# Performance work log

Measured on AMD Instinct MI355X. Metric: run time of the kernel, lower is better.

## Reference

```python
import jax, jax.numpy as jnp
import numpy as np

B, N, DIM, H, K = 2, 8192, 256, 8, 32
HD = DIM // H


def setup_inputs() -> dict:
    key = jax.random.key(0)
    ks = jax.random.split(key, 10)
    s = 1.0 / np.sqrt(DIM)
    return {
        "x": jax.random.normal(ks[0], (B, N, DIM), jnp.float32),
        "xyz": jax.random.normal(ks[1], (B, N, 3), jnp.float32),
        "idx": jax.random.randint(ks[2], (B, N, K), 0, N, jnp.int32),
        "Wq": jax.random.normal(ks[3], (DIM, DIM), jnp.float32) * s,
        "bq": jnp.zeros((DIM,), jnp.float32),
        "Wk": jax.random.normal(ks[4], (DIM, DIM), jnp.float32) * s,
        "bk": jnp.zeros((DIM,), jnp.float32),
        "Wv": jax.random.normal(ks[5], (DIM, DIM), jnp.float32) * s,
        "bv": jnp.zeros((DIM,), jnp.float32),
        "Wo": jax.random.normal(ks[6], (DIM, DIM), jnp.float32) * s,
        "bo": jnp.zeros((DIM,), jnp.float32),
        "W1": jax.random.normal(ks[7], (3, 32), jnp.float32) * 0.5,
        "b1": jnp.zeros((32,), jnp.float32),
        "W2": jax.random.normal(ks[8], (32, H), jnp.float32) * 0.2,
        "b2": jnp.zeros((H,), jnp.float32),
    }


def reference(x, xyz, idx, Wq, bq, Wk, bk, Wv, bv, Wo, bo, W1, b1, W2, b2):
    Bn, Nn, C = x.shape
    k = idx.shape[-1]
    q = (x @ Wq + bq).reshape(Bn, Nn, H, HD)          # [B,N,H,hd]
    kf = (x @ Wk + bk).reshape(Bn, Nn, H, HD)
    vf = (x @ Wv + bv).reshape(Bn, Nn, H, HD)
    # gather k neighbors per point (per-batch fancy indexing)
    gather = jax.vmap(lambda f, i: f[i])               # [N,H,hd],[N,k] -> [N,k,H,hd]
    kn = gather(kf, idx)                               # [B,N,k,H,hd]
    vn = gather(vf, idx)
    nxyz = jax.vmap(lambda p, i: p[i])(xyz, idx)       # [B,N,k,3]
    rel = xyz[:, :, None, :] - nxyz                    # [B,N,k,3]
    bias = jax.nn.relu(rel @ W1 + b1) @ W2 + b2        # [B,N,k,H]
    scores = jnp.einsum('bnhd,bnkhd->bnhk', q, kn) / np.sqrt(HD).astype(np.float32)
    scores = scores + bias.transpose(0, 1, 3, 2)       # [B,N,H,k]
    attn = jax.nn.softmax(scores, axis=-1)
    out = jnp.einsum('bnhk,bnkhd->bnhd', attn, vn).reshape(Bn, Nn, C)
    return out @ Wo + bo
```

## Files before the change

kernel.cpp:

```cpp
#include <hip/hip_runtime.h>
#include <hip/hip_bf16.h>

typedef unsigned int uint32;
typedef unsigned short ushort;
typedef __attribute__((ext_vector_type(4))) float floatx4;
typedef __attribute__((ext_vector_type(8))) __bf16 bf16x8;

#define NPTS 8192
#define HSZ 524288

__device__ __forceinline__ ushort f2bf(float f) {
    uint32 u = __float_as_uint(f);
    uint32 r = (u + 0x7fffu + ((u >> 16) & 1u)) >> 16;
    return (ushort)r;
}
__device__ __forceinline__ float bf1(ushort u) { return __uint_as_float((uint32)u << 16); }
__device__ __forceinline__ float bflo(uint32 u) { return __uint_as_float(u << 16); }
__device__ __forceinline__ float bfhi(uint32 u) { return __uint_as_float(u & 0xffff0000u); }

__global__ __launch_bounds__(256) void prep_kernel(
    const float* __restrict__ x, const float* __restrict__ xyz, const int* __restrict__ idx,
    const float* __restrict__ Wq, const float* __restrict__ Wk,
    const float* __restrict__ Wv, const float* __restrict__ Wo,
    const float* __restrict__ bq, const float* __restrict__ bk, const float* __restrict__ bv,
    const float* __restrict__ W1, const float* __restrict__ b1,
    const float* __restrict__ W2, const float* __restrict__ b2,
    ushort* __restrict__ xb, ushort* __restrict__ Wqkvt, ushort* __restrict__ Wot,
    float* __restrict__ biasqkv, ushort* __restrict__ bias_hg) {
    const int bi = blockIdx.x;
    const int tid = threadIdx.x;
    if (bi < 4096) {
        int i = (bi * 256 + tid) * 4;
        float4 v = *(const float4*)(x + i);
        ushort4 o;
        o.x = f2bf(v.x); o.y = f2bf(v.y); o.z = f2bf(v.z); o.w = f2bf(v.w);
        *(ushort4*)(xb + i) = o;
    } else if (bi < 5120) {
        int f = (bi - 4096) * 256 + tid;
        if (f < 768 * 256) {
            int n = f >> 8, k = f & 255;
            int seg = n >> 8, nc = n & 255;
            const float* W = (seg == 0) ? Wq : (seg == 1) ? Wk : Wv;
            Wqkvt[f] = f2bf(W[k * 256 + nc]);
        } else {
            int g = f - 768 * 256;
            int n = g >> 8, k = g & 255;
            Wot[g] = f2bf(Wo[k * 256 + n]);
        }
        if (f < 768) biasqkv[f] = (f < 256) ? bq[f] : (f < 512) ? bk[f - 256] : bv[f - 512];
    } else {
        __shared__ float W1s[96], b1s[32], W2s[256], b2s[8];
        if (tid < 96) W1s[tid] = W1[tid];
        if (tid < 32) b1s[tid] = b1[tid];
        W2s[tid] = W2[tid];
        if (tid < 8) b2s[tid] = b2[tid];
        __syncthreads();
        const int wid = tid >> 6, lane = tid & 63;
        const int s = lane >> 5, j = lane & 31;
        const int p = (bi - 5120) * 8 + wid * 2 + s;
        const int b = p >> 13, n = p & 8191;
        const int nj = idx[(size_t)p * 32 + j];
        const size_t pb = ((size_t)b * NPTS + n) * 3;
        const size_t nb = ((size_t)b * NPTS + nj) * 3;
        const float rx = xyz[pb + 0] - xyz[nb + 0];
        const float ry = xyz[pb + 1] - xyz[nb + 1];
        const float rz = xyz[pb + 2] - xyz[nb + 2];
        float acc[8];
#pragma unroll
        for (int h = 0; h < 8; ++h) acc[h] = b2s[h];
#pragma unroll
        for (int u = 0; u < 32; ++u) {
            float hv = rx * W1s[u] + ry * W1s[32 + u] + rz * W1s[64 + u] + b1s[u];
            hv = fmaxf(hv, 0.f);
#pragma unroll
            for (int h = 0; h < 8; ++h) acc[h] += hv * W2s[u * 8 + h];
        }
#pragma unroll
        for (int h = 0; h < 8; ++h) bias_hg[(size_t)h * HSZ + p * 32 + j] = f2bf(acc[h]);
    }
}

__global__ __launch_bounds__(256) void gemm_qkv(const ushort* __restrict__ A,
                                                const ushort* __restrict__ Wt,
                                                const float* __restrict__ bias,
                                                ushort* __restrict__ qh, ushort* __restrict__ kh,
                                                ushort* __restrict__ vh) {
    __shared__ __align__(16) ushort As[128 * 64];
    __shared__ __align__(16) ushort Bs[128 * 64];
    const int tid = threadIdx.x;
    const int w = tid >> 6, lane = tid & 63;
    const int m0 = blockIdx.y * 128, n0 = blockIdx.x * 128;
    const int wm = (w & 1) * 64, wn = (w >> 1) * 64;

    floatx4 acc[4][4] = {};

    for (int kt = 0; kt < 256; kt += 64) {
        __syncthreads();
#pragma unroll
        for (int c4 = 0; c4 < 4; ++c4) {
            const int c = w * 4 + c4;
            const int r = c * 8 + (lane >> 3);
            const int gseg = (lane & 7) ^ (r & 7);
            const char* ga = (const char*)(A + (size_t)(m0 + r) * 256 + kt) + gseg * 16;
            const char* gb = (const char*)(Wt + (size_t)(n0 + r) * 256 + kt) + gseg * 16;
            __builtin_amdgcn_global_load_lds((const __attribute__((address_space(1))) void*)ga,
                                             (__attribute__((address_space(3))) void*)((char*)As + c * 1024),
                                             16, 0, 0);
            __builtin_amdgcn_global_load_lds((const __attribute__((address_space(1))) void*)gb,
                                             (__attribute__((address_space(3))) void*)((char*)Bs + c * 1024),
                                             16, 0, 0);
        }
        __syncthreads();

        bf16x8 af[2][4], bg[2][4];
#pragma unroll
        for (int kk = 0; kk < 2; ++kk) {
            const int s = kk * 4 + (lane >> 4);
            const int phys = s ^ (lane & 7);
#pragma unroll
            for (int i = 0; i < 4; ++i) {
                af[kk][i] = *(const bf16x8*)((const char*)As + (wm + i * 16 + (lane & 15)) * 128 + phys * 16);
                bg[kk][i] = *(const bf16x8*)((const char*)Bs + (wn + i * 16 + (lane & 15)) * 128 + phys * 16);
            }
        }
#pragma unroll
        for (int kk = 0; kk < 2; ++kk)
#pragma unroll
            for (int mi = 0; mi < 4; ++mi)
#pragma unroll
                for (int ni = 0; ni < 4; ++ni)
                    acc[mi][ni] = __builtin_amdgcn_mfma_f32_16x16x32_bf16(af[kk][mi], bg[kk][ni], acc[mi][ni], 0, 0, 0);
    }

#pragma unroll
    for (int ni = 0; ni < 4; ++ni) {
        const int col = n0 + wn + ni * 16 + (lane & 15);
        const int seg = col >> 8;
        const int head = (col >> 5) & 7;
        const int dim = col & 31;
        ushort* segp = (seg == 0) ? qh : (seg == 1) ? kh : vh;
        const float bv = bias[col];
#pragma unroll
        for (int mi = 0; mi < 4; ++mi) {
            const int row0 = m0 + wm + mi * 16 + (lane >> 4) * 4;
#pragma unroll
            for (int r = 0; r < 4; ++r)
                segp[(size_t)head * HSZ + (size_t)(row0 + r) * 32 + dim] = f2bf(acc[mi][ni][r] + bv);
        }
    }
}

__global__ __launch_bounds__(256) void gemm_mfma64(const ushort* __restrict__ A,
                                                   const ushort* __restrict__ Wt,
                                                   const float* __restrict__ bias,
                                                   float* __restrict__ outv, int N) {
    __shared__ __align__(16) ushort As[64 * 32];
    __shared__ __align__(16) ushort Bs[64 * 32];
    const int tid = threadIdx.x;
    const int w = tid >> 6, lane = tid & 63;
    const int m0 = blockIdx.y * 64, n0 = blockIdx.x * 64;
    const int row = tid >> 2;
    const int col16 = (tid & 3) * 16;

    floatx4 acc[4] = {};

    for (int kt = 0; kt < 256; kt += 32) {
        __syncthreads();
        {
            const char* ga = (const char*)(A + (size_t)(m0 + row) * 256 + kt) + col16;
            const char* gb = (const char*)(Wt + (size_t)(n0 + row) * 256 + kt) + col16;
            __builtin_amdgcn_global_load_lds((const __attribute__((address_space(1))) void*)ga,
                                             (__attribute__((address_space(3))) void*)((char*)As + w * 1024),
                                             16, 0, 0);
            __builtin_amdgcn_global_load_lds((const __attribute__((address_space(1))) void*)gb,
                                             (__attribute__((address_space(3))) void*)((char*)Bs + w * 1024),
                                             16, 0, 0);
        }
        __syncthreads();

        bf16x8 af = *(const bf16x8*)&As[(w * 16 + (lane & 15)) * 32 + (lane >> 4) * 8];
        bf16x8 bg[4];
#pragma unroll
        for (int ni = 0; ni < 4; ++ni)
            bg[ni] = *(const bf16x8*)&Bs[(ni * 16 + (lane & 15)) * 32 + (lane >> 4) * 8];
#pragma unroll
        for (int ni = 0; ni < 4; ++ni)
            acc[ni] = __builtin_amdgcn_mfma_f32_16x16x32_bf16(af, bg[ni], acc[ni], 0, 0, 0);
    }

#pragma unroll
    for (int ni = 0; ni < 4; ++ni) {
        const int col = n0 + ni * 16 + (lane & 15);
        const float bv = bias[col];
        const int row0 = m0 + w * 16 + (lane >> 4) * 4;
#pragma unroll
        for (int r = 0; r < 4; ++r)
            outv[(size_t)(row0 + r) * N + col] = acc[ni][r] + bv;
    }
}

__global__ __launch_bounds__(256) void attn_kernel(
    const ushort* __restrict__ qh, const ushort* __restrict__ kh, const ushort* __restrict__ vh,
    const int* __restrict__ idx, const ushort* __restrict__ bias_hg, ushort* __restrict__ out) {
    __shared__ __align__(16) float q_s[4][2][32];
    __shared__ float e_s[4][2][32];
    __shared__ uint32 off_s[4][2][32];
    __shared__ float ssum_s[4][2];

    const int tid = threadIdx.x, wid = tid >> 6, lane = tid & 63;
    const int h = blockIdx.x >> 11;
    const int pg = blockIdx.x & 2047;
    const int pbase = pg * 8 + wid * 2;

    const char* kh_h = (const char*)(kh + (size_t)h * HSZ);
    const char* vh_h = (const char*)(vh + (size_t)h * HSZ);

    const int s = lane >> 5, j = lane & 31;
    const int p = pbase + s;
    const int b = p >> 13;

    off_s[wid][s][j] = (uint32)(idx[(size_t)p * 32 + j] + b * NPTS) * 64u;
    q_s[wid][s][j] = bf1(qh[(size_t)h * HSZ + p * 32 + j]);
    __syncthreads();

    {
        const uint4* kp = (const uint4*)(kh_h + off_s[wid][s][j]);
        float d = 0.f;
#pragma unroll
        for (int c = 0; c < 4; ++c) {
            uint4 kv = kp[c];
            float4 qa = *(const float4*)&q_s[wid][s][c * 8];
            float4 qb = *(const float4*)&q_s[wid][s][c * 8 + 4];
            d += bflo(kv.x) * qa.x + bfhi(kv.x) * qa.y
               + bflo(kv.y) * qa.z + bfhi(kv.y) * qa.w
               + bflo(kv.z) * qb.x + bfhi(kv.z) * qb.y
               + bflo(kv.w) * qb.z + bfhi(kv.w) * qb.w;
        }
        const float sc = d * 0.17677669529663687f + bf1(bias_hg[(size_t)h * HSZ + p * 32 + j]);
        const float e = __expf(sc);
        float ssum = e;
#pragma unroll
        for (int msk = 16; msk >= 1; msk >>= 1) ssum += __shfl_xor(ssum, msk, 64);
        e_s[wid][s][j] = e;
        if (j == 0) ssum_s[wid][s] = ssum;
    }
    __syncthreads();

    {
        const int s2 = lane >> 5, hj = (lane >> 4) & 1, d2 = lane & 15;
        const int p2 = pbase + s2;
        const float rinv = __builtin_amdgcn_rcpf(ssum_s[wid][s2]);
        float ax = 0.f, ay = 0.f;
#pragma unroll
        for (int jj = 0; jj < 16; ++jj) {
            const int j2 = hj * 16 + jj;
            const float wgt = e_s[wid][s2][j2];
            const uint32 v = *(const uint32*)(vh_h + off_s[wid][s2][j2] + d2 * 4);
            ax += wgt * bflo(v);
            ay += wgt * bfhi(v);
        }
        ax += __shfl_xor(ax, 16, 64);
        ay += __shfl_xor(ay, 16, 64);
        if (hj == 0) {
            const uint32 o = (uint32)f2bf(ax * rinv) | ((uint32)f2bf(ay * rinv) << 16);
            *(uint32*)(out + (size_t)p2 * 256 + h * 32 + d2 * 2) = o;
        }
    }
}

extern "C" void kernel_launch(void* const* d_in, const int* in_sizes, int n_in,
                              void* d_out, int out_size, void* d_ws, size_t ws_size,
                              hipStream_t stream) {
    const float* x   = (const float*)d_in[0];
    const float* xyz = (const float*)d_in[1];
    const int*   idx = (const int*)d_in[2];
    const float* Wq = (const float*)d_in[3];
    const float* bq = (const float*)d_in[4];
    const float* Wk = (const float*)d_in[5];
    const float* bk = (const float*)d_in[6];
    const float* Wv = (const float*)d_in[7];
    const float* bv = (const float*)d_in[8];
    const float* Wo = (const float*)d_in[9];
    const float* bo = (const float*)d_in[10];
    const float* W1 = (const float*)d_in[11];
    const float* b1 = (const float*)d_in[12];
    const float* W2 = (const float*)d_in[13];
    const float* b2 = (const float*)d_in[14];

    char* wsb = (char*)d_ws;
    ushort* x_bf    = (ushort*)wsb;
    ushort* aout_bf = x_bf;
    ushort* qh      = (ushort*)(wsb + 8388608);
    ushort* kh      = (ushort*)(wsb + 16777216);
    ushort* vh      = (ushort*)(wsb + 25165824);
    ushort* bias_hg = (ushort*)(wsb + 33554432);
    ushort* Wqkvt   = (ushort*)(wsb + 41943040);
    ushort* Wot     = (ushort*)(wsb + 42336256);
    float*  biasqkv = (float*)(wsb + 42467328);

    prep_kernel<<<7168, 256, 0, stream>>>(x, xyz, idx, Wq, Wk, Wv, Wo, bq, bk, bv,
                                          W1, b1, W2, b2, x_bf, Wqkvt, Wot, biasqkv, bias_hg);

    gemm_qkv<<<dim3(6, 128), 256, 0, stream>>>(x_bf, Wqkvt, biasqkv, qh, kh, vh);

    attn_kernel<<<16384, 256, 0, stream>>>(qh, kh, vh, idx, bias_hg, aout_bf);

    gemm_mfma64<<<dim3(4, 256), 256, 0, stream>>>(aout_bf, Wot, bo, (float*)d_out, 256);
}
```

Baseline: 182.5 us.

## Vectorize V gather with 16-byte loads and shuffle reduce-scatter; drop block barriers

The attention kernel's value gather is remapped so each lane loads 16 bytes (8 bf16) of a neighbor's V row for 4 neighbors, instead of 4 bytes for 16 neighbors. The partial sums are then combined across lanes with a butterfly of xor-shuffles that also scatters the output dimensions. Neighbor offsets and exp weights are packed into one uint2 LDS array. The softmax sum is kept in registers, which lets both __syncthreads be removed because all shared data is produced and consumed within a single wavefront. This trades fewer, wider gather transactions and less synchronization for extra shuffle and select work. It relies on wave-local LDS ordering without an explicit barrier or fence.

```diff
diff --git a/kernel.cpp b/kernel.cpp
--- a/kernel.cpp
+++ b/kernel.cpp
@@ -203,9 +203,7 @@
     const ushort* __restrict__ qh, const ushort* __restrict__ kh, const ushort* __restrict__ vh,
     const int* __restrict__ idx, const ushort* __restrict__ bias_hg, ushort* __restrict__ out) {
     __shared__ __align__(16) float q_s[4][2][32];
-    __shared__ float e_s[4][2][32];
-    __shared__ uint32 off_s[4][2][32];
-    __shared__ float ssum_s[4][2];
+    __shared__ __align__(8) uint2 oe_s[4][2][32];
 
     const int tid = threadIdx.x, wid = tid >> 6, lane = tid & 63;
     const int h = blockIdx.x >> 11;
@@ -219,12 +217,13 @@
     const int p = pbase + s;
     const int b = p >> 13;
 
-    off_s[wid][s][j] = (uint32)(idx[(size_t)p * 32 + j] + b * NPTS) * 64u;
+    const uint32 off = (uint32)(idx[(size_t)p * 32 + j] + b * NPTS) * 64u;
+    oe_s[wid][s][j].x = off;
     q_s[wid][s][j] = bf1(qh[(size_t)h * HSZ + p * 32 + j]);
-    __syncthreads();
-
+
+    float rinv;
     {
-        const uint4* kp = (const uint4*)(kh_h + off_s[wid][s][j]);
+        const uint4* kp = (const uint4*)(kh_h + off);
         float d = 0.f;
 #pragma unroll
         for (int c = 0; c < 4; ++c) {
@@ -238,32 +237,54 @@
         }
         const float sc = d * 0.17677669529663687f + bf1(bias_hg[(size_t)h * HSZ + p * 32 + j]);
         const float e = __expf(sc);
+        oe_s[wid][s][j].y = __float_as_uint(e);
         float ssum = e;
 #pragma unroll
         for (int msk = 16; msk >= 1; msk >>= 1) ssum += __shfl_xor(ssum, msk, 64);
-        e_s[wid][s][j] = e;
-        if (j == 0) ssum_s[wid][s] = ssum;
-    }
-    __syncthreads();
+        rinv = __builtin_amdgcn_rcpf(ssum);
+    }
 
     {
-        const int s2 = lane >> 5, hj = (lane >> 4) & 1, d2 = lane & 15;
-        const int p2 = pbase + s2;
-        const float rinv = __builtin_amdgcn_rcpf(ssum_s[wid][s2]);
-        float ax = 0.f, ay = 0.f;
-#pragma unroll
-        for (int jj = 0; jj < 16; ++jj) {
-            const int j2 = hj * 16 + jj;
-            const float wgt = e_s[wid][s2][j2];
-            const uint32 v = *(const uint32*)(vh_h + off_s[wid][s2][j2] + d2 * 4);
-            ax += wgt * bflo(v);
-            ay += wgt * bfhi(v);
-        }
-        ax += __shfl_xor(ax, 16, 64);
-        ay += __shfl_xor(ay, 16, 64);
-        if (hj == 0) {
-            const uint32 o = (uint32)f2bf(ax * rinv) | ((uint32)f2bf(ay * rinv) << 16);
-            *(uint32*)(out + (size_t)p2 * 256 + h * 32 + d2 * 2) = o;
+        const int q4 = lane & 3, g = (lane >> 2) & 7;
+        const char* vbase = vh_h + q4 * 16;
+        float a0 = 0.f, a1 = 0.f, a2 = 0.f, a3 = 0.f, a4 = 0.f, a5 = 0.f, a6 = 0.f, a7 = 0.f;
+#pragma unroll
+        for (int i = 0; i < 4; ++i) {
+            const uint2 oe = oe_s[wid][s][g * 4 + i];
+            const float wgt = __uint_as_float(oe.y);
+            const uint4 v = *(const uint4*)(vbase + oe.x);
+            a0 += wgt * bflo(v.x); a1 += wgt * bfhi(v.x);
+            a2 += wgt * bflo(v.y); a3 += wgt * bfhi(v.y);
+            a4 += wgt * bflo(v.z); a5 += wgt * bfhi(v.z);
+            a6 += wgt * bflo(v.w); a7 += wgt * bfhi(v.w);
+        }
+        const bool hi4 = (lane & 4) != 0;
+        {
+            float t0 = hi4 ? a0 : a4, t1 = hi4 ? a1 : a5, t2 = hi4 ? a2 : a6, t3 = hi4 ? a3 : a7;
+            float k0 = hi4 ? a4 : a0, k1 = hi4 ? a5 : a1, k2 = hi4 ? a6 : a2, k3 = hi4 ? a7 : a3;
+            a0 = k0 + __shfl_xor(t0, 4, 64);
+            a1 = k1 + __shfl_xor(t1, 4, 64);
+            a2 = k2 + __shfl_xor(t2, 4, 64);
+            a3 = k3 + __shfl_xor(t3, 4, 64);
+        }
+        const bool hi8 = (lane & 8) != 0;
+        {
+            float t0 = hi8 ? a0 : a2, t1 = hi8 ? a1 : a3;
+            float k0 = hi8 ? a2 : a0, k1 = hi8 ? a3 : a1;
+            a0 = k0 + __shfl_xor(t0, 8, 64);
+            a1 = k1 + __shfl_xor(t1, 8, 64);
+        }
+        const bool hi16 = (lane & 16) != 0;
+        {
+            float t0 = hi16 ? a0 : a1;
+            float k0 = hi16 ? a1 : a0;
+            a0 = k0 + __shfl_xor(t0, 16, 64);
+        }
+        const uint32 u = (uint32)f2bf(a0 * rinv);
+        const uint32 up = (uint32)__shfl_xor((int)u, 16, 64);
+        if (!hi16) {
+            const int D = q4 * 8 + (hi4 ? 4 : 0) + (hi8 ? 2 : 0);
+            *(uint32*)(out + (size_t)p * 256 + h * 32 + D) = u | (up << 16);
         }
     }
 }
```

After: 181.0 us. Within noise of the previous version (-0.8%).
